# Kernel optimization log

Hardware: AMD Instinct MI355X
Metric: run time of the kernel (lower is better)

## Reference

```python
import jax, jax.numpy as jnp
import numpy as np

N, E, D, D_OUT = 100000, 3200000, 64, 64
EPS = 1e-5


def setup_inputs() -> dict:
    key = jax.random.key(0)
    ks = jax.random.split(key, 16)
    s = 1.0 / np.sqrt(D)
    inp = {
        "x": jax.random.normal(ks[0], (N, D), dtype=jnp.float32),
        "edge_index": jax.random.randint(ks[1], (2, E), 0, N, dtype=jnp.int64),
        # layer 1: GCNConv weight/bias, fc weight/bias, BN gamma/beta
        "W1": jax.random.uniform(ks[2], (D, D), jnp.float32, -s, s),
        "b1": jnp.zeros((D,), jnp.float32),
        "fw1": jax.random.uniform(ks[3], (D, D), jnp.float32, -s, s),
        "fb1": jax.random.uniform(ks[4], (D,), jnp.float32, -s, s),
        "g1": jnp.ones((D,), jnp.float32),
        "bt1": jnp.zeros((D,), jnp.float32),
        # layer 2
        "W2": jax.random.uniform(ks[5], (D, D), jnp.float32, -s, s),
        "b2": jnp.zeros((D,), jnp.float32),
        "fw2": jax.random.uniform(ks[6], (D, D_OUT), jnp.float32, -s, s),
        "fb2": jax.random.uniform(ks[7], (D_OUT,), jnp.float32, -s, s),
        "g2": jnp.ones((D_OUT,), jnp.float32),
        "bt2": jnp.zeros((D_OUT,), jnp.float32),
    }
    return inp


def _gcn_conv(x, W, b, src, dst, dinv):
    # x' = X W, then symmetric-normalized scatter-add aggregation (self loops included)
    h = x @ W                                   # [N, D]
    msg = (dinv[src] * dinv[dst])[:, None] * h[src]  # [E+N, D]
    out = jax.ops.segment_sum(msg, dst, num_segments=N)
    return out + b


def _fc_bn_relu(x, fw, fb, g, bt):
    y = x @ fw + fb
    mu = jnp.mean(y, axis=0)
    var = jnp.mean((y - mu) ** 2, axis=0)  # biased var (torch BN training mode)
    y = (y - mu) * jax.lax.rsqrt(var + EPS) * g + bt
    return jax.nn.relu(y)


def reference(x, edge_index, W1, b1, fw1, fb1, g1, bt1, W2, b2, fw2, fb2, g2, bt2):
    loop = jnp.arange(N, dtype=edge_index.dtype)
    src = jnp.concatenate([edge_index[0], loop])  # add self loops
    dst = jnp.concatenate([edge_index[1], loop])
    deg = jax.ops.segment_sum(jnp.ones_like(dst, dtype=x.dtype), dst, num_segments=N)
    dinv = jax.lax.rsqrt(deg)  # deg >= 1 thanks to self loops

    h = _gcn_conv(x, W1, b1, src, dst, dinv)
    h = _fc_bn_relu(h, fw1, fb1, g1, bt1)
    h = _gcn_conv(h, W2, b2, src, dst, dinv)
    h = _fc_bn_relu(h, fw2, fb2, g2, bt2)
    return h
```

## Files before the change

### kernel.cpp

```cpp
#include <hip/hip_runtime.h>

#define N_NODES 100000
#define N_EDGES 3200000
#define D 64
#define EPS 1e-5f

#define BSHIFT 7
#define BNODES 128
#define NBUCK ((N_NODES + BNODES - 1) / BNODES)
#define P1_CHUNK 4096
#define NB_P1 ((N_EDGES + P1_CHUNK - 1) / P1_CHUNK)
#define SRC_MASK 0x1FFFFu
#define BCAP 4480
#define TBL_STRIDE 784

typedef __attribute__((ext_vector_type(8))) short bf16x8;
typedef __attribute__((ext_vector_type(4))) float f32x4;

__device__ __forceinline__ unsigned short f2bf(float f) {
  unsigned int u = __float_as_uint(f);
  u += 0x7FFFu + ((u >> 16) & 1u);
  return (unsigned short)(u >> 16);
}
__device__ __forceinline__ float bf2f(unsigned short h) {
  return __uint_as_float(((unsigned int)h) << 16);
}
__device__ __forceinline__ float2 bfpair(unsigned int u) {
  return make_float2(__uint_as_float(u << 16), __uint_as_float(u & 0xFFFF0000u));
}
__device__ __forceinline__ void addp(float2 a[4], uint4 u) {
  a[0] += bfpair(u.x);
  a[1] += bfpair(u.y);
  a[2] += bfpair(u.z);
  a[3] += bfpair(u.w);
}

__global__ __launch_bounds__(256) void combine_weights(
    const float* __restrict__ W1, const float* __restrict__ b1,
    const float* __restrict__ fw1, const float* __restrict__ fb1,
    const float* __restrict__ W2, const float* __restrict__ b2,
    const float* __restrict__ fw2, const float* __restrict__ fb2,
    unsigned int* __restrict__ WcB1, float* __restrict__ bc1,
    unsigned int* __restrict__ WcB2, float* __restrict__ bc2,
    float* __restrict__ stats) {
  if (blockIdx.x == 2) {
    if (threadIdx.x < 256) stats[threadIdx.x] = 0.0f;
    return;
  }
  const float* W  = blockIdx.x ? W2  : W1;
  const float* fw = blockIdx.x ? fw2 : fw1;
  const float* b  = blockIdx.x ? b2  : b1;
  const float* fb = blockIdx.x ? fb2 : fb1;
  unsigned int* WcB = blockIdx.x ? WcB2 : WcB1;
  float* bc = blockIdx.x ? bc2 : bc1;

  __shared__ float sW[64 * 64];
  __shared__ float sf[64 * 64];
  __shared__ float sC[64 * 64];
  for (int i = threadIdx.x; i < 4096; i += 256) { sW[i] = W[i]; sf[i] = fw[i]; }
  __syncthreads();
  for (int o = threadIdx.x; o < 4096; o += 256) {
    int i = o >> 6, j = o & 63;
    float acc = 0.f;
    #pragma unroll
    for (int k = 0; k < 64; ++k) acc += sW[i * 64 + k] * sf[k * 64 + j];
    sC[o] = acc;
  }
  __syncthreads();
  for (int o = threadIdx.x; o < 2048; o += 256) {
    int jj = o & 3, L = (o >> 2) & 63, kh = (o >> 8) & 1, nt = o >> 9;
    int k0 = (L >> 4) * 8 + jj * 2 + kh * 32;
    int n  = nt * 16 + (L & 15);
    unsigned int lo = f2bf(sC[k0 * 64 + n]);
    unsigned int hi = f2bf(sC[(k0 + 1) * 64 + n]);
    WcB[o] = (hi << 16) | lo;
  }
  if (threadIdx.x < 64) {
    int j = threadIdx.x;
    float acc = fb[j];
    #pragma unroll
    for (int k = 0; k < 64; ++k) acc += b[k] * sf[k * 64 + j];
    bc[j] = acc;
  }
}

__global__ __launch_bounds__(256) void pass1_sort(
    const int* __restrict__ src, const int* __restrict__ dst,
    unsigned int* __restrict__ stage, unsigned short* __restrict__ tbl) {
  __shared__ unsigned int hist[NBUCK];
  __shared__ unsigned int ts[256];
  __shared__ unsigned int sorted[P1_CHUNK];
  const int tid = threadIdx.x;
  const int e0 = blockIdx.x * P1_CHUNK;

  for (int b = tid; b < NBUCK; b += 256) hist[b] = 0;
  __syncthreads();

  int dreg[16];
  #pragma unroll
  for (int k = 0; k < 16; ++k) {
    int e = e0 + k * 256 + tid;
    int d = (e < N_EDGES) ? dst[e] : -1;
    dreg[k] = d;
    if (d >= 0) atomicAdd(&hist[((unsigned)d) >> BSHIFT], 1u);
  }
  __syncthreads();

  unsigned int v[4], run = 0;
  #pragma unroll
  for (int j = 0; j < 4; ++j) {
    int bk = 4 * tid + j;
    unsigned int h = (bk < NBUCK) ? hist[bk] : 0u;
    v[j] = run;
    run += h;
  }
  ts[tid] = run;
  __syncthreads();
  for (int o = 1; o < 256; o <<= 1) {
    unsigned int add = (tid >= o) ? ts[tid - o] : 0u;
    __syncthreads();
    ts[tid] += add;
    __syncthreads();
  }
  const unsigned int excl = ts[tid] - run;
  const unsigned int m = ts[255];
  unsigned short* trow = tbl + (size_t)blockIdx.x * TBL_STRIDE;
  #pragma unroll
  for (int j = 0; j < 4; ++j) {
    int bk = 4 * tid + j;
    if (bk < NBUCK) {
      unsigned int o = excl + v[j];
      hist[bk] = o;
      trow[bk] = (unsigned short)o;
    }
  }
  if (tid == 0) trow[NBUCK] = (unsigned short)m;
  __syncthreads();

  #pragma unroll
  for (int k = 0; k < 16; ++k) {
    int e = e0 + k * 256 + tid;
    int t = dreg[k];
    if (t >= 0) {
      unsigned int pos = atomicAdd(&hist[((unsigned)t) >> BSHIFT], 1u);
      sorted[pos] = (((unsigned)(t & (BNODES - 1))) << 17) | (unsigned)src[e];
    }
  }
  __syncthreads();

  unsigned int* so = stage + (size_t)blockIdx.x * P1_CHUNK;
  for (int i = tid; i < (int)m; i += 256) so[i] = sorted[i];
}

__global__ __launch_bounds__(512) void pass2_sort(
    const unsigned int* __restrict__ stage, const unsigned short* __restrict__ tbl,
    int* __restrict__ eSrc, int* __restrict__ off, int* __restrict__ edeg,
    float* __restrict__ dinv, const float* __restrict__ x,
    unsigned short* __restrict__ Xs) {
  __shared__ int spre[512];
  __shared__ int cnt[BNODES];
  __shared__ int ts[BNODES];
  __shared__ float dinvL[BNODES];
  __shared__ unsigned int raw[BCAP];
  __shared__ int sorted[BCAP];
  const int b = blockIdx.x, tid = threadIdx.x;
  const int n0 = b * BNODES;

  int base0 = 0, base1 = 0, len0 = 0, len1 = 0;
  {
    int s0 = 2 * tid, s1 = 2 * tid + 1;
    if (s0 < NB_P1) {
      const unsigned short* trow = tbl + (size_t)s0 * TBL_STRIDE;
      int o0 = trow[b], o1 = trow[b + 1];
      base0 = s0 * P1_CHUNK + o0;
      len0 = o1 - o0;
    }
    if (s1 < NB_P1) {
      const unsigned short* trow = tbl + (size_t)s1 * TBL_STRIDE;
      int o0 = trow[b], o1 = trow[b + 1];
      base1 = s1 * P1_CHUNK + o0;
      len1 = o1 - o0;
    }
  }
  if (tid < BNODES) cnt[tid] = 0;
  const int mylen = len0 + len1;
  spre[tid] = mylen;
  __syncthreads();
  for (int o = 1; o < 512; o <<= 1) {
    int add = (tid >= o) ? spre[tid - o] : 0;
    __syncthreads();
    spre[tid] += add;
    __syncthreads();
  }
  const int m = spre[511];
  const int pref = spre[tid] - mylen;

  for (int j = 0; j < len0; ++j) {
    unsigned int p = stage[base0 + j];
    raw[pref + j] = p;
    atomicAdd(&cnt[p >> 17], 1);
  }
  for (int j = 0; j < len1; ++j) {
    unsigned int p = stage[base1 + j];
    raw[pref + len0 + j] = p;
    atomicAdd(&cnt[p >> 17], 1);
  }
  __syncthreads();

  int v = 0;
  if (tid < BNODES) { v = cnt[tid]; ts[tid] = v; }
  __syncthreads();
  for (int o = 1; o < BNODES; o <<= 1) {
    int add = (tid >= o && tid < BNODES) ? ts[tid - o] : 0;
    __syncthreads();
    if (tid < BNODES) ts[tid] += add;
    __syncthreads();
  }
  if (tid < BNODES) {
    int excl = ts[tid] - v;
    int node = n0 + tid;
    float dv = rsqrtf((float)v + 1.0f);
    dinvL[tid] = dv;
    if (node < N_NODES) {
      off[node]  = b * BCAP + excl;
      edeg[node] = v;
      dinv[node] = dv;
    }
    cnt[tid] = excl;
  }
  __syncthreads();

  for (int i = tid; i < m; i += 512) {
    unsigned int p = raw[i];
    int pos = atomicAdd(&cnt[p >> 17], 1);
    if (pos < BCAP) sorted[pos] = (int)(p & SRC_MASK);
  }
  __syncthreads();

  int* out = eSrc + (size_t)b * BCAP;
  for (int i = tid; i < m; i += 512) out[i] = sorted[i];

  const int rows = min(BNODES, N_NODES - n0);
  for (int i = tid; i < rows * 64; i += 512) {
    int r = i >> 6;
    size_t g = (size_t)(n0 + r) * 64 + (i & 63);
    Xs[g] = f2bf(dinvL[r] * x[g]);
  }
}

__global__ __launch_bounds__(256) void agg_csr(
    const int* __restrict__ off, const int* __restrict__ edeg,
    const int* __restrict__ eSrc, const unsigned short* __restrict__ Xs,
    const float* __restrict__ dinv, unsigned short* __restrict__ agg) {
  const int wid = (blockIdx.x * 256 + threadIdx.x) >> 6;
  const int lane = threadIdx.x & 63;
  const int grp = lane >> 3, sub = lane & 7;
  if (wid >= N_NODES) return;
  const int s0 = off[wid];
  const int s1 = s0 + edeg[wid];
  const uint4* XsV = (const uint4*)Xs;

  float2 acc[4];
  {
    uint4 u = XsV[(size_t)wid * 8 + sub];
    if (grp != 0) { u.x = 0; u.y = 0; u.z = 0; u.w = 0; }
    acc[0] = bfpair(u.x);
    acc[1] = bfpair(u.y);
    acc[2] = bfpair(u.z);
    acc[3] = bfpair(u.w);
  }

  int e = s0;
  const int eend = s1 - ((s1 - s0) & 31);
  for (; e < eend; e += 32) {
    int sa = eSrc[e + grp];
    int sb = eSrc[e + 8 + grp];
    int sc = eSrc[e + 16 + grp];
    int sd = eSrc[e + 24 + grp];
    uint4 ua = XsV[(size_t)sa * 8 + sub];
    uint4 ub = XsV[(size_t)sb * 8 + sub];
    uint4 uc = XsV[(size_t)sc * 8 + sub];
    uint4 ud = XsV[(size_t)sd * 8 + sub];
    addp(acc, ua); addp(acc, ub); addp(acc, uc); addp(acc, ud);
  }
  if (e < s1) {
    const int lim = s1 - 1;
    int ea = e + grp, eb = e + 8 + grp, ec = e + 16 + grp, ed = e + 24 + grp;
    int sa = eSrc[min(ea, lim)];
    int sb = eSrc[min(eb, lim)];
    int sc = eSrc[min(ec, lim)];
    int sd = eSrc[min(ed, lim)];
    uint4 ua = XsV[(size_t)sa * 8 + sub];
    uint4 ub = XsV[(size_t)sb * 8 + sub];
    uint4 uc = XsV[(size_t)sc * 8 + sub];
    uint4 ud = XsV[(size_t)sd * 8 + sub];
    if (ea > lim) { ua.x = 0; ua.y = 0; ua.z = 0; ua.w = 0; }
    if (eb > lim) { ub.x = 0; ub.y = 0; ub.z = 0; ub.w = 0; }
    if (ec > lim) { uc.x = 0; uc.y = 0; uc.z = 0; uc.w = 0; }
    if (ed > lim) { ud.x = 0; ud.y = 0; ud.z = 0; ud.w = 0; }
    addp(acc, ua); addp(acc, ub); addp(acc, uc); addp(acc, ud);
  }

  #pragma unroll
  for (int mk = 8; mk <= 32; mk <<= 1) {
    #pragma unroll
    for (int i = 0; i < 4; ++i) {
      acc[i].x += __shfl_xor(acc[i].x, mk, 64);
      acc[i].y += __shfl_xor(acc[i].y, mk, 64);
    }
  }

  if (grp == 0) {
    float dt = dinv[wid];
    uint4 o;
    o.x = ((unsigned)f2bf(acc[0].y * dt) << 16) | f2bf(acc[0].x * dt);
    o.y = ((unsigned)f2bf(acc[1].y * dt) << 16) | f2bf(acc[1].x * dt);
    o.z = ((unsigned)f2bf(acc[2].y * dt) << 16) | f2bf(acc[2].x * dt);
    o.w = ((unsigned)f2bf(acc[3].y * dt) << 16) | f2bf(acc[3].x * dt);
    *(uint4*)(agg + (size_t)wid * 64 + sub * 8) = o;
  }
}

__global__ __launch_bounds__(256) void gemm_stats(
    const unsigned short* __restrict__ A, const unsigned int* __restrict__ WcB,
    const float* __restrict__ bc, unsigned short* __restrict__ Yb,
    float* __restrict__ colsum, float* __restrict__ colsq) {
  const int tid = threadIdx.x;
  const int L = tid & 63, wv = tid >> 6;
  const int quad = L >> 4, l16 = L & 15;

  const bf16x8* Wv = (const bf16x8*)WcB;
  bf16x8 bfr[4][2];
  #pragma unroll
  for (int nt = 0; nt < 4; ++nt)
    #pragma unroll
    for (int kh = 0; kh < 2; ++kh)
      bfr[nt][kh] = Wv[(nt * 2 + kh) * 64 + L];
  float bcv[4];
  #pragma unroll
  for (int nt = 0; nt < 4; ++nt) bcv[nt] = bc[nt * 16 + l16];

  const bf16x8* Av = (const bf16x8*)A;
  float psum[4] = {0.f, 0.f, 0.f, 0.f}, psq[4] = {0.f, 0.f, 0.f, 0.f};

  #pragma unroll
  for (int loop = 0; loop < 2; ++loop) {
    const int rowbase = blockIdx.x * 128 + loop * 64 + wv * 16;
    const int m = min(rowbase + l16, N_NODES - 1);
    bf16x8 a0 = Av[(size_t)m * 8 + quad];
    bf16x8 a1 = Av[(size_t)m * 8 + 4 + quad];
    #pragma unroll
    for (int nt = 0; nt < 4; ++nt) {
      f32x4 acc = {0.f, 0.f, 0.f, 0.f};
      acc = __builtin_amdgcn_mfma_f32_16x16x32_bf16(a0, bfr[nt][0], acc, 0, 0, 0);
      acc = __builtin_amdgcn_mfma_f32_16x16x32_bf16(a1, bfr[nt][1], acc, 0, 0, 0);
      #pragma unroll
      for (int r = 0; r < 4; ++r) {
        int row = rowbase + quad * 4 + r;
        if (row < N_NODES) {
          float y = acc[r] + bcv[nt];
          Yb[(size_t)row * 64 + nt * 16 + l16] = f2bf(y);
          psum[nt] += y;
          psq[nt] += y * y;
        }
      }
    }
  }

  #pragma unroll
  for (int nt = 0; nt < 4; ++nt) {
    psum[nt] += __shfl_xor(psum[nt], 16, 64);
    psum[nt] += __shfl_xor(psum[nt], 32, 64);
    psq[nt]  += __shfl_xor(psq[nt], 16, 64);
    psq[nt]  += __shfl_xor(psq[nt], 32, 64);
  }
  __shared__ float rsum[4][64];
  __shared__ float rsq[4][64];
  if (L < 16) {
    #pragma unroll
    for (int nt = 0; nt < 4; ++nt) {
      rsum[wv][nt * 16 + L] = psum[nt];
      rsq[wv][nt * 16 + L]  = psq[nt];
    }
  }
  __syncthreads();
  if (tid < 64) {
    float s = rsum[0][tid] + rsum[1][tid] + rsum[2][tid] + rsum[3][tid];
    float q = rsq[0][tid] + rsq[1][tid] + rsq[2][tid] + rsq[3][tid];
    atomicAdd(&colsum[tid], s);
    atomicAdd(&colsq[tid], q);
  }
}

__global__ __launch_bounds__(256) void prescale_y(
    unsigned short* __restrict__ YbXs, const float* __restrict__ dinv,
    const float* __restrict__ colsum, const float* __restrict__ colsq,
    const float* __restrict__ g, const float* __restrict__ bt) {
  __shared__ float sa[64], sc[64];
  if (threadIdx.x < 64) {
    int j = threadIdx.x;
    float mu = colsum[j] * (1.0f / N_NODES);
    float var = colsq[j] * (1.0f / N_NODES) - mu * mu;
    float s = rsqrtf(var + EPS) * g[j];
    sa[j] = s;
    sc[j] = bt[j] - mu * s;
  }
  __syncthreads();
  int idx = blockIdx.x * blockDim.x + threadIdx.x;
  if (idx < N_NODES * D) {
    int i = idx >> 6, j = idx & 63;
    float y = bf2f(YbXs[idx]);
    YbXs[idx] = f2bf(dinv[i] * fmaxf(fmaf(y, sa[j], sc[j]), 0.f));
  }
}

__global__ __launch_bounds__(256) void final_norm(
    const unsigned short* __restrict__ Yb, float* __restrict__ out,
    const float* __restrict__ colsum, const float* __restrict__ colsq,
    const float* __restrict__ g, const float* __restrict__ bt) {
  __shared__ float sa[64], sc[64];
  if (threadIdx.x < 64) {
    int j = threadIdx.x;
    float mu = colsum[j] * (1.0f / N_NODES);
    float var = colsq[j] * (1.0f / N_NODES) - mu * mu;
    float s = rsqrtf(var + EPS) * g[j];
    sa[j] = s;
    sc[j] = bt[j] - mu * s;
  }
  __syncthreads();
  int idx = blockIdx.x * blockDim.x + threadIdx.x;
  if (idx < N_NODES * D) {
    int j = idx & 63;
    out[idx] = fmaxf(fmaf(bf2f(Yb[idx]), sa[j], sc[j]), 0.f);
  }
}

extern "C" void kernel_launch(void* const* d_in, const int* in_sizes, int n_in,
                              void* d_out, int out_size, void* d_ws, size_t ws_size,
                              hipStream_t stream) {
  const float* x   = (const float*)d_in[0];
  const int*   src = (const int*)d_in[1];
  const int*   dst = src + N_EDGES;
  const float* W1  = (const float*)d_in[2];
  const float* b1  = (const float*)d_in[3];
  const float* fw1 = (const float*)d_in[4];
  const float* fb1 = (const float*)d_in[5];
  const float* g1  = (const float*)d_in[6];
  const float* bt1 = (const float*)d_in[7];
  const float* W2  = (const float*)d_in[8];
  const float* b2  = (const float*)d_in[9];
  const float* fw2 = (const float*)d_in[10];
  const float* fb2 = (const float*)d_in[11];
  const float* g2  = (const float*)d_in[12];
  const float* bt2 = (const float*)d_in[13];

  float* out = (float*)d_out;

  unsigned char* w = (unsigned char*)d_ws;
  unsigned int*   stage = (unsigned int*)w;
  unsigned short* aggb  = (unsigned short*)w;
  size_t ofs = ((size_t)NB_P1 * P1_CHUNK * 4 + 255) & ~(size_t)255;
  float*          dinv  = (float*)(w + ofs);
  unsigned short* XsYb  = (unsigned short*)(dinv + N_NODES);
  int*            eSrc  = (int*)(XsYb + (size_t)N_NODES * D);
  int*            off   = eSrc + (size_t)NBUCK * BCAP;
  int*            edeg  = off + N_NODES;
  unsigned short* tbl   = (unsigned short*)(edeg + N_NODES);
  unsigned int* WcB1 = (unsigned int*)(tbl + (size_t)NB_P1 * TBL_STRIDE);
  float* bc1  = (float*)(WcB1 + 2048);
  unsigned int* WcB2 = (unsigned int*)(bc1 + 64);
  float* bc2  = (float*)(WcB2 + 2048);
  float* sum1 = bc2 + 64;
  float* sq1  = sum1 + 64;
  float* sum2 = sq1 + 64;
  float* sq2  = sum2 + 64;

  const int nd = N_NODES * D;
  dim3 blk(256);

  combine_weights<<<3, blk, 0, stream>>>(W1, b1, fw1, fb1, W2, b2, fw2, fb2,
                                         WcB1, bc1, WcB2, bc2, sum1);

  pass1_sort<<<NB_P1, blk, 0, stream>>>(src, dst, stage, tbl);
  pass2_sort<<<NBUCK, 512, 0, stream>>>(stage, tbl, eSrc, off, edeg, dinv, x, XsYb);

  agg_csr<<<(nd + 255) / 256, blk, 0, stream>>>(off, edeg, eSrc, XsYb, dinv, aggb);
  gemm_stats<<<(N_NODES + 127) / 128, blk, 0, stream>>>(aggb, WcB1, bc1, XsYb, sum1, sq1);

  prescale_y<<<(nd + 255) / 256, blk, 0, stream>>>(XsYb, dinv, sum1, sq1, g1, bt1);
  agg_csr<<<(nd + 255) / 256, blk, 0, stream>>>(off, edeg, eSrc, XsYb, dinv, aggb);
  gemm_stats<<<(N_NODES + 127) / 128, blk, 0, stream>>>(aggb, WcB2, bc2, XsYb, sum2, sq2);

  final_norm<<<(nd + 255) / 256, blk, 0, stream>>>(XsYb, out, sum2, sq2, g2, bt2);
}
```

Measured before the change: 342.5 us.

## Fuse GEMM, batch-norm and ReLU using a grid-wide barrier; merge weight combine into sort

```diff
diff --git a/kernel.cpp b/kernel.cpp
--- a/kernel.cpp
+++ b/kernel.cpp
@@ -13,6 +13,7 @@
 #define SRC_MASK 0x1FFFFu
 #define BCAP 4480
 #define TBL_STRIDE 784
+#define NGB ((N_NODES + 127) / 128)
 
 typedef __attribute__((ext_vector_type(8))) short bf16x8;
 typedef __attribute__((ext_vector_type(4))) float f32x4;
@@ -35,65 +36,60 @@
   a[3] += bfpair(u.w);
 }
 
-__global__ __launch_bounds__(256) void combine_weights(
+__global__ __launch_bounds__(256) void pass1_sort(
+    const int* __restrict__ src, const int* __restrict__ dst,
+    unsigned int* __restrict__ stage, unsigned short* __restrict__ tbl,
     const float* __restrict__ W1, const float* __restrict__ b1,
     const float* __restrict__ fw1, const float* __restrict__ fb1,
     const float* __restrict__ W2, const float* __restrict__ b2,
     const float* __restrict__ fw2, const float* __restrict__ fb2,
     unsigned int* __restrict__ WcB1, float* __restrict__ bc1,
-    unsigned int* __restrict__ WcB2, float* __restrict__ bc2,
-    float* __restrict__ stats) {
-  if (blockIdx.x == 2) {
-    if (threadIdx.x < 256) stats[threadIdx.x] = 0.0f;
+    unsigned int* __restrict__ WcB2, float* __restrict__ bc2) {
+  __shared__ union {
+    struct { unsigned int hist[NBUCK]; unsigned int ts[256]; unsigned int sorted[P1_CHUNK]; } p;
+    struct { float sW[4096]; float sfT[65 * 64]; } c;
+  } sm;
+  const int tid = threadIdx.x;
+
+  if (blockIdx.x >= NB_P1) {
+    const int layer = blockIdx.x - NB_P1;
+    const float* W  = layer ? W2  : W1;
+    const float* fw = layer ? fw2 : fw1;
+    const float* b  = layer ? b2  : b1;
+    const float* fb = layer ? fb2 : fb1;
+    unsigned int* WcB = layer ? WcB2 : WcB1;
+    float* bc = layer ? bc2 : bc1;
+
+    for (int i = tid; i < 4096; i += 256) {
+      sm.c.sW[i] = W[i];
+      int t = i >> 6, n = i & 63;
+      sm.c.sfT[n * 65 + t] = fw[i];
+    }
+    __syncthreads();
+    for (int o = tid; o < 2048; o += 256) {
+      int jj = o & 3, L = (o >> 2) & 63, kh = (o >> 8) & 1, nt = o >> 9;
+      int k0 = (L >> 4) * 8 + jj * 2 + kh * 32;
+      int n  = nt * 16 + (L & 15);
+      float d0 = 0.f, d1 = 0.f;
+      #pragma unroll
+      for (int t = 0; t < 64; ++t) {
+        float f = sm.c.sfT[n * 65 + t];
+        d0 += sm.c.sW[k0 * 64 + t] * f;
+        d1 += sm.c.sW[(k0 + 1) * 64 + t] * f;
+      }
+      WcB[o] = ((unsigned)f2bf(d1) << 16) | f2bf(d0);
+    }
+    if (tid < 64) {
+      float acc = fb[tid];
+      #pragma unroll
+      for (int k = 0; k < 64; ++k) acc += b[k] * sm.c.sfT[tid * 65 + k];
+      bc[tid] = acc;
+    }
     return;
   }
-  const float* W  = blockIdx.x ? W2  : W1;
-  const float* fw = blockIdx.x ? fw2 : fw1;
-  const float* b  = blockIdx.x ? b2  : b1;
-  const float* fb = blockIdx.x ? fb2 : fb1;
-  unsigned int* WcB = blockIdx.x ? WcB2 : WcB1;
-  float* bc = blockIdx.x ? bc2 : bc1;
-
-  __shared__ float sW[64 * 64];
-  __shared__ float sf[64 * 64];
-  __shared__ float sC[64 * 64];
-  for (int i = threadIdx.x; i < 4096; i += 256) { sW[i] = W[i]; sf[i] = fw[i]; }
-  __syncthreads();
-  for (int o = threadIdx.x; o < 4096; o += 256) {
-    int i = o >> 6, j = o & 63;
-    float acc = 0.f;
-    #pragma unroll
-    for (int k = 0; k < 64; ++k) acc += sW[i * 64 + k] * sf[k * 64 + j];
-    sC[o] = acc;
-  }
-  __syncthreads();
-  for (int o = threadIdx.x; o < 2048; o += 256) {
-    int jj = o & 3, L = (o >> 2) & 63, kh = (o >> 8) & 1, nt = o >> 9;
-    int k0 = (L >> 4) * 8 + jj * 2 + kh * 32;
-    int n  = nt * 16 + (L & 15);
-    unsigned int lo = f2bf(sC[k0 * 64 + n]);
-    unsigned int hi = f2bf(sC[(k0 + 1) * 64 + n]);
-    WcB[o] = (hi << 16) | lo;
-  }
-  if (threadIdx.x < 64) {
-    int j = threadIdx.x;
-    float acc = fb[j];
-    #pragma unroll
-    for (int k = 0; k < 64; ++k) acc += b[k] * sf[k * 64 + j];
-    bc[j] = acc;
-  }
-}
-
-__global__ __launch_bounds__(256) void pass1_sort(
-    const int* __restrict__ src, const int* __restrict__ dst,
-    unsigned int* __restrict__ stage, unsigned short* __restrict__ tbl) {
-  __shared__ unsigned int hist[NBUCK];
-  __shared__ unsigned int ts[256];
-  __shared__ unsigned int sorted[P1_CHUNK];
-  const int tid = threadIdx.x;
+
   const int e0 = blockIdx.x * P1_CHUNK;
-
-  for (int b = tid; b < NBUCK; b += 256) hist[b] = 0;
+  for (int b = tid; b < NBUCK; b += 256) sm.p.hist[b] = 0;
   __syncthreads();
 
   int dreg[16];
@@ -102,7 +98,7 @@
     int e = e0 + k * 256 + tid;
     int d = (e < N_EDGES) ? dst[e] : -1;
     dreg[k] = d;
-    if (d >= 0) atomicAdd(&hist[((unsigned)d) >> BSHIFT], 1u);
+    if (d >= 0) atomicAdd(&sm.p.hist[((unsigned)d) >> BSHIFT], 1u);
   }
   __syncthreads();
 
@@ -110,27 +106,27 @@
   #pragma unroll
   for (int j = 0; j < 4; ++j) {
     int bk = 4 * tid + j;
-    unsigned int h = (bk < NBUCK) ? hist[bk] : 0u;
+    unsigned int h = (bk < NBUCK) ? sm.p.hist[bk] : 0u;
     v[j] = run;
     run += h;
   }
-  ts[tid] = run;
+  sm.p.ts[tid] = run;
   __syncthreads();
   for (int o = 1; o < 256; o <<= 1) {
-    unsigned int add = (tid >= o) ? ts[tid - o] : 0u;
-    __syncthreads();
-    ts[tid] += add;
-    __syncthreads();
-  }
-  const unsigned int excl = ts[tid] - run;
-  const unsigned int m = ts[255];
+    unsigned int add = (tid >= o) ? sm.p.ts[tid - o] : 0u;
+    __syncthreads();
+    sm.p.ts[tid] += add;
+    __syncthreads();
+  }
+  const unsigned int excl = sm.p.ts[tid] - run;
+  const unsigned int m = sm.p.ts[255];
   unsigned short* trow = tbl + (size_t)blockIdx.x * TBL_STRIDE;
   #pragma unroll
   for (int j = 0; j < 4; ++j) {
     int bk = 4 * tid + j;
     if (bk < NBUCK) {
       unsigned int o = excl + v[j];
-      hist[bk] = o;
+      sm.p.hist[bk] = o;
       trow[bk] = (unsigned short)o;
     }
   }
@@ -142,21 +138,21 @@
     int e = e0 + k * 256 + tid;
     int t = dreg[k];
     if (t >= 0) {
-      unsigned int pos = atomicAdd(&hist[((unsigned)t) >> BSHIFT], 1u);
-      sorted[pos] = (((unsigned)(t & (BNODES - 1))) << 17) | (unsigned)src[e];
+      unsigned int pos = atomicAdd(&sm.p.hist[((unsigned)t) >> BSHIFT], 1u);
+      sm.p.sorted[pos] = (((unsigned)(t & (BNODES - 1))) << 17) | (unsigned)src[e];
     }
   }
   __syncthreads();
 
   unsigned int* so = stage + (size_t)blockIdx.x * P1_CHUNK;
-  for (int i = tid; i < (int)m; i += 256) so[i] = sorted[i];
+  for (int i = tid; i < (int)m; i += 256) so[i] = sm.p.sorted[i];
 }
 
 __global__ __launch_bounds__(512) void pass2_sort(
     const unsigned int* __restrict__ stage, const unsigned short* __restrict__ tbl,
     int* __restrict__ eSrc, int* __restrict__ off, int* __restrict__ edeg,
     float* __restrict__ dinv, const float* __restrict__ x,
-    unsigned short* __restrict__ Xs) {
+    unsigned short* __restrict__ Xs, int* __restrict__ zeroRegion) {
   __shared__ int spre[512];
   __shared__ int cnt[BNODES];
   __shared__ int ts[BNODES];
@@ -165,6 +161,8 @@
   __shared__ int sorted[BCAP];
   const int b = blockIdx.x, tid = threadIdx.x;
   const int n0 = b * BNODES;
+
+  if (b == 0 && tid < 258) zeroRegion[tid] = 0;
 
   int base0 = 0, base1 = 0, len0 = 0, len1 = 0;
   {
@@ -321,10 +319,13 @@
   }
 }
 
-__global__ __launch_bounds__(256) void gemm_stats(
+__global__ __launch_bounds__(256, 4) void gemm_fused(
     const unsigned short* __restrict__ A, const unsigned int* __restrict__ WcB,
-    const float* __restrict__ bc, unsigned short* __restrict__ Yb,
-    float* __restrict__ colsum, float* __restrict__ colsq) {
+    const float* __restrict__ bc, const float* __restrict__ g,
+    const float* __restrict__ bt, const float* __restrict__ dinv,
+    float* __restrict__ colsum, float* __restrict__ colsq,
+    int* __restrict__ ctr, unsigned short* __restrict__ outb,
+    float* __restrict__ outf, const int mode) {
   const int tid = threadIdx.x;
   const int L = tid & 63, wv = tid >> 6;
   const int quad = L >> 4, l16 = L & 15;
@@ -341,6 +342,7 @@
   for (int nt = 0; nt < 4; ++nt) bcv[nt] = bc[nt * 16 + l16];
 
   const bf16x8* Av = (const bf16x8*)A;
+  float y[2][4][4];
   float psum[4] = {0.f, 0.f, 0.f, 0.f}, psq[4] = {0.f, 0.f, 0.f, 0.f};
 
   #pragma unroll
@@ -357,11 +359,11 @@
       #pragma unroll
       for (int r = 0; r < 4; ++r) {
         int row = rowbase + quad * 4 + r;
+        float yy = acc[r] + bcv[nt];
+        y[loop][nt][r] = yy;
         if (row < N_NODES) {
-          float y = acc[r] + bcv[nt];
-          Yb[(size_t)row * 64 + nt * 16 + l16] = f2bf(y);
-          psum[nt] += y;
-          psq[nt] += y * y;
+          psum[nt] += yy;
+          psq[nt] += yy * yy;
         }
       }
     }
@@ -390,48 +392,49 @@
     atomicAdd(&colsum[tid], s);
     atomicAdd(&colsq[tid], q);
   }
-}
-
-__global__ __launch_bounds__(256) void prescale_y(
-    unsigned short* __restrict__ YbXs, const float* __restrict__ dinv,
-    const float* __restrict__ colsum, const float* __restrict__ colsq,
-    const float* __restrict__ g, const float* __restrict__ bt) {
-  __shared__ float sa[64], sc[64];
-  if (threadIdx.x < 64) {
-    int j = threadIdx.x;
-    float mu = colsum[j] * (1.0f / N_NODES);
-    float var = colsq[j] * (1.0f / N_NODES) - mu * mu;
-    float s = rsqrtf(var + EPS) * g[j];
-    sa[j] = s;
-    sc[j] = bt[j] - mu * s;
-  }
-  __syncthreads();
-  int idx = blockIdx.x * blockDim.x + threadIdx.x;
-  if (idx < N_NODES * D) {
-    int i = idx >> 6, j = idx & 63;
-    float y = bf2f(YbXs[idx]);
-    YbXs[idx] = f2bf(dinv[i] * fmaxf(fmaf(y, sa[j], sc[j]), 0.f));
-  }
-}
-
-__global__ __launch_bounds__(256) void final_norm(
-    const unsigned short* __restrict__ Yb, float* __restrict__ out,
-    const float* __restrict__ colsum, const float* __restrict__ colsq,
-    const float* __restrict__ g, const float* __restrict__ bt) {
-  __shared__ float sa[64], sc[64];
-  if (threadIdx.x < 64) {
-    int j = threadIdx.x;
-    float mu = colsum[j] * (1.0f / N_NODES);
-    float var = colsq[j] * (1.0f / N_NODES) - mu * mu;
-    float s = rsqrtf(var + EPS) * g[j];
-    sa[j] = s;
-    sc[j] = bt[j] - mu * s;
-  }
-  __syncthreads();
-  int idx = blockIdx.x * blockDim.x + threadIdx.x;
-  if (idx < N_NODES * D) {
-    int j = idx & 63;
-    out[idx] = fmaxf(fmaf(bf2f(Yb[idx]), sa[j], sc[j]), 0.f);
+
+  __syncthreads();
+  if (tid == 0) {
+    __threadfence();
+    atomicAdd(ctr, 1);
+    while (__hip_atomic_load(ctr, __ATOMIC_RELAXED, __HIP_MEMORY_SCOPE_AGENT)
+           < (int)gridDim.x)
+      __builtin_amdgcn_s_sleep(8);
+    __threadfence();
+  }
+  __syncthreads();
+
+  float av[4], cv[4];
+  #pragma unroll
+  for (int nt = 0; nt < 4; ++nt) {
+    int j = nt * 16 + l16;
+    float s = __hip_atomic_load(&colsum[j], __ATOMIC_RELAXED, __HIP_MEMORY_SCOPE_AGENT);
+    float q = __hip_atomic_load(&colsq[j], __ATOMIC_RELAXED, __HIP_MEMORY_SCOPE_AGENT);
+    float mu = s * (1.0f / N_NODES);
+    float var = q * (1.0f / N_NODES) - mu * mu;
+    float aa = rsqrtf(var + EPS) * g[j];
+    av[nt] = aa;
+    cv[nt] = bt[j] - mu * aa;
+  }
+
+  #pragma unroll
+  for (int loop = 0; loop < 2; ++loop) {
+    #pragma unroll
+    for (int r = 0; r < 4; ++r) {
+      int row = blockIdx.x * 128 + loop * 64 + wv * 16 + quad * 4 + r;
+      if (row < N_NODES) {
+        float dv = (mode == 0) ? dinv[row] : 1.0f;
+        #pragma unroll
+        for (int nt = 0; nt < 4; ++nt) {
+          float t = fmaxf(fmaf(y[loop][nt][r], av[nt], cv[nt]), 0.f);
+          int col = nt * 16 + l16;
+          if (mode == 0)
+            outb[(size_t)row * 64 + col] = f2bf(t * dv);
+          else
+            outf[(size_t)row * 64 + col] = t;
+        }
+      }
+    }
   }
 }
 
@@ -474,22 +477,20 @@
   float* sq1  = sum1 + 64;
   float* sum2 = sq1 + 64;
   float* sq2  = sum2 + 64;
+  int*   ctr  = (int*)(sq2 + 64);
 
   const int nd = N_NODES * D;
   dim3 blk(256);
 
-  combine_weights<<<3, blk, 0, stream>>>(W1, b1, fw1, fb1, W2, b2, fw2, fb2,
-                                         WcB1, bc1, WcB2, bc2, sum1);
-
-  pass1_sort<<<NB_P1, blk, 0, stream>>>(src, dst, stage, tbl);
-  pass2_sort<<<NBUCK, 512, 0, stream>>>(stage, tbl, eSrc, off, edeg, dinv, x, XsYb);
-
+  pass1_sort<<<NB_P1 + 2, blk, 0, stream>>>(src, dst, stage, tbl,
+                                            W1, b1, fw1, fb1, W2, b2, fw2, fb2,
+                                            WcB1, bc1, WcB2, bc2);
+  pass2_sort<<<NBUCK, 512, 0, stream>>>(stage, tbl, eSrc, off, edeg, dinv, x,
+                                        XsYb, (int*)sum1);
   agg_csr<<<(nd + 255) / 256, blk, 0, stream>>>(off, edeg, eSrc, XsYb, dinv, aggb);
-  gemm_stats<<<(N_NODES + 127) / 128, blk, 0, stream>>>(aggb, WcB1, bc1, XsYb, sum1, sq1);
-
-  prescale_y<<<(nd + 255) / 256, blk, 0, stream>>>(XsYb, dinv, sum1, sq1, g1, bt1);
+  gemm_fused<<<NGB, blk, 0, stream>>>(aggb, WcB1, bc1, g1, bt1, dinv,
+                                      sum1, sq1, &ctr[0], XsYb, out, 0);
   agg_csr<<<(nd + 255) / 256, blk, 0, stream>>>(off, edeg, eSrc, XsYb, dinv, aggb);
-  gemm_stats<<<(N_NODES + 127) / 128, blk, 0, stream>>>(aggb, WcB2, bc2, XsYb, sum2, sq2);
-
-  final_norm<<<(nd + 255) / 256, blk, 0, stream>>>(XsYb, out, sum2, sq2, g2, bt2);
-}
+  gemm_fused<<<NGB, blk, 0, stream>>>(aggb, WcB2, bc2, g2, bt2, dinv,
+                                      sum2, sq2, &ctr[1], XsYb, out, 1);
+}
```

New measurement: 421.4 us. +23.0%, slower.
